# Kernel optimization log

Hardware: AMD Instinct MI355X
Metric: run time of the kernel (lower is better)

The kernel has to match this reference:

```python
import jax, jax.numpy as jnp
import numpy as np


def _centers(n):
    # make_coord_3d: cell-center coordinates in (-1, 1)
    r = 1.0 / n
    return -1.0 + r + 2.0 * r * jnp.arange(n, dtype=jnp.float32)


def setup_inputs() -> dict:
    key = jax.random.key(0)
    ks = jax.random.split(key, 16)
    B, C, Tin, Hin, Win = 1, 64, 6, 40, 40
    Gc = 27 + 8 * C  # 539 channels into conv00_3d
    s = lambda k, shp: jax.random.normal(k, shp, dtype=jnp.float32) * 0.05
    return {
        "feat": jax.random.normal(ks[0], (B, C, Tin, Hin, Win), dtype=jnp.float32),
        # conv00_3d = depthwise(1x1x1, groups=Gc) + pointwise(Gc->256)
        "dw1_w": s(ks[1], (Gc,)), "dw1_b": s(ks[2], (Gc,)),
        "pw1_w": s(ks[3], (256, Gc)), "pw1_b": s(ks[4], (256,)),
        "fc1_w": s(ks[5], (256, 256)), "fc1_b": s(ks[6], (256,)),
        "fc2_w": s(ks[7], (3, 256)), "fc2_b": s(ks[8], (3,)),
        # short_cut = depthwise(1x1x1, groups=C) + pointwise(C->3)
        "sc_dw_w": s(ks[9], (C,)), "sc_dw_b": s(ks[10], (C,)),
        "sc_pw_w": s(ks[11], (3, C)), "sc_pw_b": s(ks[12], (3,)),
        "T_out": 12, "H_out": 80, "W_out": 80,
    }


def _pw(x, w, b):
    # 1x1x1 Conv3d
    return jnp.einsum('bcthw,oc->bothw', x, w) + b[None, :, None, None, None]


def _forward(feat, dw1_w, dw1_b, pw1_w, pw1_b, fc1_w, fc1_b, fc2_w, fc2_b,
             sc_dw_w, sc_dw_b, sc_pw_w, sc_pw_b, T_out, H_out, W_out):
    B, C, Tin, Hin, Win = feat.shape
    ct, ch, cw = _centers(T_out), _centers(H_out), _centers(W_out)  # target centers
    lt, lh, lw = _centers(Tin), _centers(Hin), _centers(Win)        # low-res centers
    rt, rx, ry = 1.0 / Tin, 1.0 / Hin, 1.0 / Win                    # 2/N/2 radii
    eps = 1e-6

    def near(c, n):
        # grid_sample nearest, align_corners=False; coords pre-clamped as in torch code
        cc = jnp.clip(c, -1.0 + 1e-6, 1.0 - 1e-6)
        return jnp.clip(jnp.round(((cc + 1.0) * n - 1.0) / 2.0), 0, n - 1).astype(jnp.int32)

    rel_coords, feat_s, areas = [], [], []
    for vt in (-1.0, 1.0):
        for vx in (-1.0, 1.0):
            for vy in (-1.0, 1.0):
                it = near(ct + vt * rt + eps, Tin)   # [T'] (separable per-dim)
                ih = near(ch + vx * rx + eps, Hin)   # [H']
                iw = near(cw + vy * ry + eps, Win)   # [W']
                f = feat[:, :, it[:, None, None], ih[None, :, None], iw[None, None, :]]
                dct = (ct - lt[it]) * Tin
                dch = (ch - lh[ih]) * Hin
                dcw = (cw - lw[iw]) * Win
                rel = jnp.stack([
                    jnp.broadcast_to(dct[:, None, None], (T_out, H_out, W_out)),
                    jnp.broadcast_to(dch[None, :, None], (T_out, H_out, W_out)),
                    jnp.broadcast_to(dcw[None, None, :], (T_out, H_out, W_out)),
                ], axis=0)
                rel = jnp.broadcast_to(rel[None], (B, 3, T_out, H_out, W_out))
                area = (jnp.abs(dct)[:, None, None] * jnp.abs(dch)[None, :, None]
                        * jnp.abs(dcw)[None, None, :]) + 1e-9
                rel_coords.append(rel)
                feat_s.append(f)
                areas.append(area)

    tot = sum(areas)
    areas_sw = areas[::-1]  # pairwise swaps 0<->7, 1<->6, 2<->5, 3<->4
    feat_s = [f * (a / tot)[None, None] for f, a in zip(feat_s, areas_sw)]

    # rel_cell: (2/size * scale) * in_size == 2.0 on every axis
    rel_cell = jnp.full((B, 3, T_out, H_out, W_out), 2.0, dtype=feat.dtype)

    grid = jnp.concatenate([*rel_coords, *feat_s, rel_cell], axis=1)  # [B,27+8C,T',H',W']

    x = _pw(grid * dw1_w[None, :, None, None, None] + dw1_b[None, :, None, None, None],
            pw1_w, pw1_b)
    ret = _pw(jax.nn.gelu(_pw(x, fc1_w, fc1_b), approximate=False), fc2_w, fc2_b)

    # short cut: depthwise-separable 1x1x1 conv, then trilinear grid_sample (border pad)
    sc = _pw(feat * sc_dw_w[None, :, None, None, None] + sc_dw_b[None, :, None, None, None],
             sc_pw_w, sc_pw_b)

    def lin_idx(c, n):
        x = jnp.clip(((c + 1.0) * n - 1.0) / 2.0, 0.0, n - 1.0)  # border padding: clip coord
        x0 = jnp.floor(x)
        frac = x - x0
        i0 = x0.astype(jnp.int32)
        i1 = jnp.minimum(i0 + 1, n - 1)
        return i0, i1, frac

    t0, t1, ft = lin_idx(ct, Tin)
    h0, h1, fh = lin_idx(ch, Hin)
    w0, w1, fw = lin_idx(cw, Win)
    g = sc[:, :, t0] * (1 - ft)[None, None, :, None, None] + sc[:, :, t1] * ft[None, None, :, None, None]
    g = g[:, :, :, h0] * (1 - fh)[None, None, None, :, None] + g[:, :, :, h1] * fh[None, None, None, :, None]
    g = g[:, :, :, :, w0] * (1 - fw) + g[:, :, :, :, w1] * fw
    return ret + g


def reference(feat, dw1_w, dw1_b, pw1_w, pw1_b, fc1_w, fc1_b, fc2_w, fc2_b,
              sc_dw_w, sc_dw_b, sc_pw_w, sc_pw_b, T_out, H_out, W_out):
    return _forward(feat, dw1_w, dw1_b, pw1_w, pw1_b, fc1_w, fc1_b, fc2_w, fc2_b,
                    sc_dw_w, sc_dw_b, sc_pw_w, sc_pw_b, T_out, H_out, W_out)
```

## Files before the change

kernel.cpp:

```cpp
#include <hip/hip_runtime.h>
#include <hip/hip_bf16.h>

using bf16 = __hip_bfloat16;
typedef __attribute__((ext_vector_type(8))) short short8x;
typedef __attribute__((ext_vector_type(4))) short short4x;
typedef __attribute__((ext_vector_type(4))) unsigned short ushort4x;
typedef __attribute__((ext_vector_type(4))) float f32x4;

__device__ __forceinline__ float b2f(bf16 x) { return __bfloat162float(x); }
__device__ __forceinline__ bf16  f2b(float x) { return __float2bfloat16(x); }
__device__ __forceinline__ short bbits(float x) { bf16 b = f2b(x); short s; __builtin_memcpy(&s, &b, 2); return s; }
__device__ __forceinline__ float bu2f(unsigned short s) {
    unsigned v = ((unsigned)s) << 16; float f; __builtin_memcpy(&f, &v, 4); return f;
}
__device__ __forceinline__ float ldin(const void* p, int i, int f32) {
    return f32 ? ((const float*)p)[i] : b2f(((const bf16*)p)[i]);
}

#define TI 6
#define HI 40
#define WI 40
#define TO 12
#define HO 80
#define WO 80
#define NIN (TI*HI*WI)
#define NOUT (TO*HO*WO)

#define F_B1    0
#define F_ACO   (F_B1 + 256)
#define F_SCW   (F_ACO + 6*256)
#define F_SCB   (F_SCW + 3*64)
#define F_SC    (F_SCB + 4)
#define F_DT    (F_SC + 3*NIN)
#define F_DH    (F_DT + 2*TO)
#define F_DW    (F_DH + 2*HO)
#define F_FT    (F_DW + 2*WO)
#define F_FH    (F_FT + TO)
#define F_FW    (F_FH + HO)
#define F_FC1B  (F_FW + WO)
#define F_FC2W  (F_FC1B + 256)
#define F_FC2B  (F_FC2W + 768)
#define F_END   (F_FC2B + 4)
#define I_IT    0
#define I_IH    (I_IT + 2*TO)
#define I_IW    (I_IH + 2*HO)
#define I_LT0   (I_IW + 2*WO)
#define I_LT1   (I_LT0 + TO)
#define I_LH0   (I_LT1 + TO)
#define I_LH1   (I_LH0 + HO)
#define I_LW0   (I_LH1 + HO)
#define I_LW1   (I_LW0 + WO)
#define I_FLAG  (I_LW1 + WO)
#define I_END   (I_FLAG + 1)

#define MPOS 32
#define ZPAD 264
#define FT_S 72

__device__ __forceinline__ void axis_tables(int i, int n_out, int n_in,
                                            float* dvals, int* ivals,
                                            int* l0, int* l1, float* fr) {
    const float r_out = 1.0f / (float)n_out;
    const float r_in  = 1.0f / (float)n_in;
    const float c = -1.0f + r_out + 2.0f * r_out * (float)i;
    #pragma unroll
    for (int v = 0; v < 2; ++v) {
        const float vv = v ? 1.0f : -1.0f;
        float cc = c + vv * r_in + 1e-6f;
        cc = fminf(fmaxf(cc, -1.0f + 1e-6f), 1.0f - 1e-6f);
        float fx = rintf(((cc + 1.0f) * (float)n_in - 1.0f) * 0.5f);
        fx = fminf(fmaxf(fx, 0.0f), (float)(n_in - 1));
        const int idx = (int)fx;
        const float l = -1.0f + r_in + 2.0f * r_in * (float)idx;
        dvals[v * n_out + i] = (c - l) * (float)n_in;
        ivals[v * n_out + i] = idx;
    }
    float x = fminf(fmaxf(((c + 1.0f) * (float)n_in - 1.0f) * 0.5f, 0.0f), (float)(n_in - 1));
    const float x0 = floorf(x);
    fr[i] = x - x0;
    const int i0 = (int)x0;
    l0[i] = i0;
    l1[i] = min(i0 + 1, n_in - 1);
}

__global__ __launch_bounds__(256)
void k_setup(const void* __restrict__ feat,
             const void* __restrict__ dw1_w, const void* __restrict__ dw1_b,
             const void* __restrict__ pw1_w, const void* __restrict__ pw1_b,
             const void* __restrict__ fc1_w, const void* __restrict__ fc1_b,
             const void* __restrict__ fc2_w, const void* __restrict__ fc2_b,
             const void* __restrict__ sc_dw_w, const void* __restrict__ sc_dw_b,
             const void* __restrict__ sc_pw_w, const void* __restrict__ sc_pw_b,
             bf16* __restrict__ fc1P, bf16* __restrict__ W1fP,
             float* __restrict__ F, int* __restrict__ I) {
    const int tid = threadIdx.x;
    const int b = blockIdx.x;
    __shared__ int sflag;
    if (tid < 64) {
        const unsigned short* u = (const unsigned short*)feat;
        const unsigned e = (u[2 * tid] >> 7) & 0xFFu;
        const unsigned long long m = __ballot(e >= 0x68u && e <= 0x8Eu);
        if (tid == 0) sflag = (__popcll(m) < 32) ? 1 : 0;
    }
    __syncthreads();
    const int f32 = sflag;

    if (b >= 288) {
        const int g = (b - 288) * 256 + tid;
        const int k = g >> 11, kc = (g >> 10) & 1, nt = (g >> 6) & 15, wl = g & 63;
        const int n = nt * 16 + (wl & 15);
        const int k0 = kc * 32 + (wl >> 4) * 8;
        bf16 v[8];
        #pragma unroll
        for (int jj = 0; jj < 8; ++jj) {
            const int ch = 24 + k * 64 + k0 + jj;
            v[jj] = f2b(ldin(pw1_w, n * 539 + ch, f32) * ldin(dw1_w, ch, f32));
        }
        *(short8x*)&W1fP[(size_t)g * 8] = *(short8x*)v;
        return;
    }
    if (b >= 256) {
        const int g = (b - 256) * 256 + tid;
        const int kc = g >> 10, nt = (g >> 6) & 15, wl = g & 63;
        const int n = nt * 16 + (wl & 15);
        const int k0 = kc * 32 + (wl >> 4) * 8;
        bf16 v[8];
        #pragma unroll
        for (int jj = 0; jj < 8; ++jj) v[jj] = f2b(ldin(fc1_w, n * 256 + k0 + jj, f32));
        *(short8x*)&fc1P[(size_t)g * 8] = *(short8x*)v;
        return;
    }

    __shared__ float row[539];
    __shared__ float red[256];
    const int o = b;

    for (int ch = tid; ch < 539; ch += 256) row[ch] = ldin(pw1_w, o * 539 + ch, f32);
    __syncthreads();

    float s = 0.f;
    for (int ch = tid; ch < 539; ch += 256) s += row[ch] * ldin(dw1_b, ch, f32);
    red[tid] = s;
    __syncthreads();
    for (int st = 128; st > 0; st >>= 1) {
        if (tid < st) red[tid] += red[tid + st];
        __syncthreads();
    }

    if (tid == 0) {
        float bacc = ldin(pw1_b, o, f32) + red[0];
        #pragma unroll
        for (int ch = 536; ch < 539; ++ch)
            bacc += 2.0f * row[ch] * ldin(dw1_w, ch, f32);
        F[F_B1 + o] = bacc;

        float A[6] = {0.f, 0.f, 0.f, 0.f, 0.f, 0.f};
        #pragma unroll
        for (int k = 0; k < 8; ++k) {
            A[(k >> 2)]           += row[3*k + 0] * ldin(dw1_w, 3*k + 0, f32);
            A[2 + ((k >> 1) & 1)] += row[3*k + 1] * ldin(dw1_w, 3*k + 1, f32);
            A[4 + (k & 1)]        += row[3*k + 2] * ldin(dw1_w, 3*k + 2, f32);
        }
        #pragma unroll
        for (int i = 0; i < 6; ++i) F[F_ACO + i * 256 + o] = A[i];
    }

    if (b == 0) {
        if (tid == 0) I[I_FLAG] = f32;
        F[F_FC1B + tid] = ldin(fc1_b, tid, f32);
        for (int r = tid; r < 768; r += 256) F[F_FC2W + r] = ldin(fc2_w, r, f32);
        if (tid < 3) F[F_FC2B + tid] = ldin(fc2_b, tid, f32);
        if (tid < 3) {
            const int j = tid;
            float sb = ldin(sc_pw_b, j, f32);
            for (int c = 0; c < 64; ++c) {
                const float pw = ldin(sc_pw_w, j * 64 + c, f32);
                F[F_SCW + j * 64 + c] = pw * ldin(sc_dw_w, c, f32);
                sb += pw * ldin(sc_dw_b, c, f32);
            }
            F[F_SCB + j] = sb;
        }
        if (tid < TO) axis_tables(tid, TO, TI, F + F_DT, I + I_IT, I + I_LT0, I + I_LT1, F + F_FT);
        if (tid < HO) axis_tables(tid, HO, HI, F + F_DH, I + I_IH, I + I_LH0, I + I_LH1, F + F_FH);
        if (tid < WO) axis_tables(tid, WO, WI, F + F_DW, I + I_IW, I + I_LW0, I + I_LW1, F + F_FW);
    }
}

__global__ __launch_bounds__(256)
void k_corner(const void* __restrict__ feat, float* __restrict__ F,
              const int* __restrict__ I, const bf16* __restrict__ W1fP,
              bf16* __restrict__ P) {
    const int tid = threadIdx.x;
    const int pt = blockIdx.x, k = blockIdx.y;
    const int pos0 = pt * 32;
    const int f32 = I[I_FLAG];

    __shared__ __align__(16) short ft[32 * FT_S];
    __shared__ __align__(16) short zt[32 * ZPAD];

    {
        const int p = tid & 31, c0 = tid >> 5;
        #pragma unroll
        for (int cc = 0; cc < 8; ++cc) {
            const int c = c0 * 8 + cc;
            ft[p * FT_S + c] = bbits(ldin(feat, c * NIN + pos0 + p, f32));
        }
    }
    __syncthreads();

    const int wl = tid & 63, w = tid >> 6;
    const int col = wl & 15, quad = wl >> 4;
    f32x4 acc[2][4] = { { {0,0,0,0},{0,0,0,0},{0,0,0,0},{0,0,0,0} },
                        { {0,0,0,0},{0,0,0,0},{0,0,0,0},{0,0,0,0} } };
    const short8x* bp = (const short8x*)W1fP;
    #pragma unroll
    for (int kc = 0; kc < 2; ++kc) {
        const short8x a0 = *(const short8x*)&ft[col * FT_S + kc * 32 + quad * 8];
        const short8x a1 = *(const short8x*)&ft[(col + 16) * FT_S + kc * 32 + quad * 8];
        #pragma unroll
        for (int nt = 0; nt < 4; ++nt) {
            const short8x bb = bp[((k * 2 + kc) * 16 + (w * 4 + nt)) * 64 + wl];
            acc[0][nt] = __builtin_amdgcn_mfma_f32_16x16x32_bf16(a0, bb, acc[0][nt], 0, 0, 0);
            acc[1][nt] = __builtin_amdgcn_mfma_f32_16x16x32_bf16(a1, bb, acc[1][nt], 0, 0, 0);
        }
    }

    if (k == 0 && tid < 96) {
        const int j = tid >> 5, p = tid & 31;
        float s = F[F_SCB + j];
        for (int c = 0; c < 64; ++c)
            s += bu2f((unsigned short)ft[p * FT_S + c]) * F[F_SCW + j * 64 + c];
        F[F_SC + j * NIN + pos0 + p] = s;
    }

    #pragma unroll
    for (int mt = 0; mt < 2; ++mt)
        #pragma unroll
        for (int nt = 0; nt < 4; ++nt) {
            const int n = w * 64 + nt * 16 + col;
            #pragma unroll
            for (int r = 0; r < 4; ++r)
                zt[(mt * 16 + quad * 4 + r) * ZPAD + n] = bbits(acc[mt][nt][r]);
        }
    __syncthreads();

    #pragma unroll
    for (int q = 0; q < 4; ++q) {
        const int i = q * 256 + tid;
        const int p = i >> 5, c8 = i & 31;
        const short8x v = *(const short8x*)&zt[p * ZPAD + c8 * 8];
        *(short8x*)(P + ((size_t)(k * NIN + pos0 + p)) * 256 + c8 * 8) = v;
    }
}

__global__ __launch_bounds__(256, 4)
void k_main(const bf16* __restrict__ P, const bf16* __restrict__ fc1P,
            const float* __restrict__ F, const int* __restrict__ I,
            void* __restrict__ outv) {
    const int tid = threadIdx.x;
    const int pos0 = blockIdx.x * MPOS;
    const int f32 = I[I_FLAG];

    __shared__ __align__(16) short zsh[MPOS * ZPAD];
    __shared__ float redc[MPOS * 4 * 3];
    __shared__ int   sh_ipos[MPOS][8];
    __shared__ float sh_wk[MPOS][8];
    __shared__ float sh_dv[MPOS][6];
    __shared__ float sh_g[3][MPOS];

    if (tid < MPOS) {
        const int p = tid;
        const int pos = pos0 + p;
        const int t = pos / (HO * WO);
        const int rem = pos - t * (HO * WO);
        const int h = rem / WO;
        const int w = rem - h * WO;
        const int   iTa[2] = { I[I_IT + t], I[I_IT + TO + t] };
        const float dTv[2] = { F[F_DT + t], F[F_DT + TO + t] };
        const int   iHa[2] = { I[I_IH + h], I[I_IH + HO + h] };
        const float dHv[2] = { F[F_DH + h], F[F_DH + HO + h] };
        const int   iWa[2] = { I[I_IW + w], I[I_IW + WO + w] };
        const float dWv[2] = { F[F_DW + w], F[F_DW + WO + w] };
        sh_dv[p][0] = dTv[0]; sh_dv[p][1] = dTv[1];
        sh_dv[p][2] = dHv[0]; sh_dv[p][3] = dHv[1];
        sh_dv[p][4] = dWv[0]; sh_dv[p][5] = dWv[1];
        const float aT[2] = { fabsf(dTv[0]), fabsf(dTv[1]) };
        const float aH[2] = { fabsf(dHv[0]), fabsf(dHv[1]) };
        const float aW[2] = { fabsf(dWv[0]), fabsf(dWv[1]) };
        const float tot = (aT[0] + aT[1]) * (aH[0] + aH[1]) * (aW[0] + aW[1]) + 8e-9f;
        #pragma unroll
        for (int k = 0; k < 8; ++k) {
            const int at = k >> 2, ah = (k >> 1) & 1, aw = k & 1;
            sh_wk[p][k] = (aT[1 - at] * aH[1 - ah] * aW[1 - aw] + 1e-9f) / tot;
            sh_ipos[p][k] = iTa[at] * (HI * WI) + iHa[ah] * WI + iWa[aw];
        }
        const int a0 = I[I_LT0 + t], a1 = I[I_LT1 + t];
        const int bh0 = I[I_LH0 + h], bh1 = I[I_LH1 + h];
        const int c0 = I[I_LW0 + w], c1 = I[I_LW1 + w];
        const float fT = F[F_FT + t], fH = F[F_FH + h], fW = F[F_FW + w];
        #pragma unroll
        for (int jj = 0; jj < 3; ++jj) {
            const float* Sj = F + F_SC + jj * NIN;
            const int i0 = a0 * (HI * WI), i1 = a1 * (HI * WI);
            const float v000 = Sj[i0 + bh0 * WI + c0], v001 = Sj[i0 + bh0 * WI + c1];
            const float v010 = Sj[i0 + bh1 * WI + c0], v011 = Sj[i0 + bh1 * WI + c1];
            const float v100 = Sj[i1 + bh0 * WI + c0], v101 = Sj[i1 + bh0 * WI + c1];
            const float v110 = Sj[i1 + bh1 * WI + c0], v111 = Sj[i1 + bh1 * WI + c1];
            const float u00 = v000 * (1.f - fT) + v100 * fT;
            const float u01 = v001 * (1.f - fT) + v101 * fT;
            const float u10 = v010 * (1.f - fT) + v110 * fT;
            const float u11 = v011 * (1.f - fT) + v111 * fT;
            const float q0 = u00 * (1.f - fH) + u10 * fH;
            const float q1 = u01 * (1.f - fH) + u11 * fH;
            sh_g[jj][p] = q0 * (1.f - fW) + q1 * fW;
        }
    }
    __syncthreads();

    {
        const int og = tid & 63, pg = tid >> 6;
        const int o4 = og * 4;
        const float4 bz = *(const float4*)&F[F_B1 + o4];
        float4 Ac[6];
        #pragma unroll
        for (int i = 0; i < 6; ++i) Ac[i] = *(const float4*)&F[F_ACO + i * 256 + o4];
        for (int pp = 0; pp < 8; ++pp) {
            const int p = pg * 8 + pp;
            float a0 = bz.x, a1 = bz.y, a2 = bz.z, a3 = bz.w;
            #pragma unroll
            for (int i = 0; i < 6; ++i) {
                const float dv = sh_dv[p][i];
                a0 += Ac[i].x * dv; a1 += Ac[i].y * dv;
                a2 += Ac[i].z * dv; a3 += Ac[i].w * dv;
            }
            #pragma unroll
            for (int k = 0; k < 8; ++k) {
                const float wk = sh_wk[p][k];
                const ushort4x u = *(const ushort4x*)(P + ((size_t)(k * NIN + sh_ipos[p][k]) * 256 + o4));
                a0 += wk * bu2f(u.x); a1 += wk * bu2f(u.y);
                a2 += wk * bu2f(u.z); a3 += wk * bu2f(u.w);
            }
            short4x zz = { bbits(a0), bbits(a1), bbits(a2), bbits(a3) };
            *(short4x*)&zsh[p * ZPAD + o4] = zz;
        }
    }
    __syncthreads();

    {
        const int wl = tid & 63, w = tid >> 6;
        const int col = wl & 15, quad = wl >> 4;
        f32x4 acc0[4] = { {0,0,0,0}, {0,0,0,0}, {0,0,0,0}, {0,0,0,0} };
        f32x4 acc1[4] = { {0,0,0,0}, {0,0,0,0}, {0,0,0,0}, {0,0,0,0} };
        const short8x* bp = (const short8x*)fc1P;
        #pragma unroll
        for (int kc = 0; kc < 8; ++kc) {
            const short8x a0 = *(const short8x*)&zsh[col * ZPAD + kc * 32 + quad * 8];
            const short8x a1 = *(const short8x*)&zsh[(col + 16) * ZPAD + kc * 32 + quad * 8];
            #pragma unroll
            for (int nt = 0; nt < 4; ++nt) {
                const short8x b = bp[(kc * 16 + w * 4 + nt) * 64 + wl];
                acc0[nt] = __builtin_amdgcn_mfma_f32_16x16x32_bf16(a0, b, acc0[nt], 0, 0, 0);
                acc1[nt] = __builtin_amdgcn_mfma_f32_16x16x32_bf16(a1, b, acc1[nt], 0, 0, 0);
            }
        }
        float part[2][3][4];
        #pragma unroll
        for (int mt = 0; mt < 2; ++mt)
            #pragma unroll
            for (int jj = 0; jj < 3; ++jj)
                #pragma unroll
                for (int r = 0; r < 4; ++r) part[mt][jj][r] = 0.f;
        #pragma unroll
        for (int nt = 0; nt < 4; ++nt) {
            const int j = w * 64 + nt * 16 + col;
            const float fb = F[F_FC1B + j];
            const float w0 = F[F_FC2W + j];
            const float w1 = F[F_FC2W + 256 + j];
            const float w2 = F[F_FC2W + 512 + j];
            #pragma unroll
            for (int r = 0; r < 4; ++r) {
                float x = acc0[nt][r] + fb;
                float hh = 0.5f * x * (1.0f + erff(x * 0.70710678118654752f));
                part[0][0][r] += w0 * hh; part[0][1][r] += w1 * hh; part[0][2][r] += w2 * hh;
                x = acc1[nt][r] + fb;
                hh = 0.5f * x * (1.0f + erff(x * 0.70710678118654752f));
                part[1][0][r] += w0 * hh; part[1][1][r] += w1 * hh; part[1][2][r] += w2 * hh;
            }
        }
        #pragma unroll
        for (int m = 1; m <= 8; m <<= 1)
            #pragma unroll
            for (int mt = 0; mt < 2; ++mt)
                #pragma unroll
                for (int jj = 0; jj < 3; ++jj)
                    #pragma unroll
                    for (int r = 0; r < 4; ++r)
                        part[mt][jj][r] += __shfl_xor(part[mt][jj][r], m, 64);
        if (col == 0) {
            #pragma unroll
            for (int mt = 0; mt < 2; ++mt)
                #pragma unroll
                for (int jj = 0; jj < 3; ++jj)
                    #pragma unroll
                    for (int r = 0; r < 4; ++r) {
                        const int p = mt * 16 + quad * 4 + r;
                        redc[(p * 4 + w) * 3 + jj] = part[mt][jj][r];
                    }
        }
    }
    __syncthreads();

    if (tid < 96) {
        const int p = tid / 3, jj = tid - 3 * p;
        float a = F[F_FC2B + jj] + sh_g[jj][p];
        #pragma unroll
        for (int w = 0; w < 4; ++w) a += redc[(p * 4 + w) * 3 + jj];
        const int oidx = jj * NOUT + pos0 + p;
        if (f32) ((float*)outv)[oidx] = a;
        else     ((bf16*)outv)[oidx] = f2b(a);
    }
}

extern "C" void kernel_launch(void* const* d_in, const int* in_sizes, int n_in,
                              void* d_out, int out_size, void* d_ws, size_t ws_size,
                              hipStream_t stream) {
    const void* feat    = d_in[0];
    const void* dw1_w   = d_in[1];
    const void* dw1_b   = d_in[2];
    const void* pw1_w   = d_in[3];
    const void* pw1_b   = d_in[4];
    const void* fc1_w   = d_in[5];
    const void* fc1_b   = d_in[6];
    const void* fc2_w   = d_in[7];
    const void* fc2_b   = d_in[8];
    const void* sc_dw_w = d_in[9];
    const void* sc_dw_b = d_in[10];
    const void* sc_pw_w = d_in[11];
    const void* sc_pw_b = d_in[12];

    const size_t P_BYTES    = (size_t)8 * NIN * 256 * 2;
    const size_t FC1P_BYTES = (size_t)256 * 256 * 2;
    const size_t W1FP_BYTES = (size_t)8 * 64 * 256 * 2;
    bf16*  P    = (bf16*)d_ws;
    bf16*  fc1P = (bf16*)((char*)d_ws + P_BYTES);
    bf16*  W1fP = (bf16*)((char*)d_ws + P_BYTES + FC1P_BYTES);
    float* F    = (float*)((char*)d_ws + P_BYTES + FC1P_BYTES + W1FP_BYTES);
    int*   I    = (int*)(F + F_END);

    k_setup<<<352, 256, 0, stream>>>(feat, dw1_w, dw1_b, pw1_w, pw1_b, fc1_w, fc1_b,
                                     fc2_w, fc2_b, sc_dw_w, sc_dw_b, sc_pw_w, sc_pw_b,
                                     fc1P, W1fP, F, I);
    k_corner<<<dim3(NIN / 32, 8), 256, 0, stream>>>(feat, F, I, W1fP, P);
    k_main<<<NOUT / MPOS, 256, 0, stream>>>(P, fc1P, F, I, (void*)d_out);
}
```

Baseline: 171.7 us.

## Shrink setup grid, widen gather loads, and use polynomial GELU approximation

Restructures the setup kernel into fewer blocks: per-output bias/coefficient rows are reduced with 16-lane shuffles instead of one block per output with a shared-memory tree, and the W1fP packing is rewritten as one contiguous 64-block range. In the main kernel, the corner gather now loads 8 bf16 channels per thread instead of 4, and the launch-bounds occupancy hint is dropped. The erff-based GELU is replaced by an Abramowitz-Stegun polynomial with a fast reciprocal and exp, which trades exactness for fewer instructions. The W1fP packing now treats the layout as one 512-row K range instead of eight 64-channel slices, which looks like it may change the indexing k_corner relies on.

```diff
diff --git a/kernel.cpp b/kernel.cpp
--- a/kernel.cpp
+++ b/kernel.cpp
@@ -3,8 +3,7 @@
 
 using bf16 = __hip_bfloat16;
 typedef __attribute__((ext_vector_type(8))) short short8x;
-typedef __attribute__((ext_vector_type(4))) short short4x;
-typedef __attribute__((ext_vector_type(4))) unsigned short ushort4x;
+typedef __attribute__((ext_vector_type(8))) unsigned short ushort8x;
 typedef __attribute__((ext_vector_type(4))) float f32x4;
 
 __device__ __forceinline__ float b2f(bf16 x) { return __bfloat162float(x); }
@@ -15,6 +14,15 @@
 }
 __device__ __forceinline__ float ldin(const void* p, int i, int f32) {
     return f32 ? ((const float*)p)[i] : b2f(((const bf16*)p)[i]);
+}
+
+__device__ __forceinline__ float gelu_f(float x) {
+    const float z = fabsf(x) * 0.70710678118654752f;
+    const float t = __builtin_amdgcn_rcpf(1.0f + 0.3275911f * z);
+    const float poly = t * (0.254829592f + t * (-0.284496736f +
+                       t * (1.421413741f + t * (-1.453152027f + t * 1.061405429f))));
+    const float erfv = 1.0f - poly * __expf(-z * z);
+    return 0.5f * x * (1.0f + copysignf(erfv, x));
 }
 
 #define TI 6
@@ -105,85 +113,72 @@
     __syncthreads();
     const int f32 = sflag;
 
-    if (b >= 288) {
-        const int g = (b - 288) * 256 + tid;
-        const int k = g >> 11, kc = (g >> 10) & 1, nt = (g >> 6) & 15, wl = g & 63;
+    if (b < 64) {
+        const int g = b * 256 + tid;
+        const int kc = g >> 10, nt = (g >> 6) & 15, wl = g & 63;
         const int n = nt * 16 + (wl & 15);
-        const int k0 = kc * 32 + (wl >> 4) * 8;
+        const int K0 = kc * 32 + (wl >> 4) * 8;
         bf16 v[8];
         #pragma unroll
         for (int jj = 0; jj < 8; ++jj) {
-            const int ch = 24 + k * 64 + k0 + jj;
+            const int ch = 24 + K0 + jj;
             v[jj] = f2b(ldin(pw1_w, n * 539 + ch, f32) * ldin(dw1_w, ch, f32));
         }
         *(short8x*)&W1fP[(size_t)g * 8] = *(short8x*)v;
         return;
     }
-    if (b >= 256) {
-        const int g = (b - 256) * 256 + tid;
+    if (b < 96) {
+        const int g = (b - 64) * 256 + tid;
         const int kc = g >> 10, nt = (g >> 6) & 15, wl = g & 63;
         const int n = nt * 16 + (wl & 15);
-        const int k0 = kc * 32 + (wl >> 4) * 8;
+        const int K0 = kc * 32 + (wl >> 4) * 8;
         bf16 v[8];
         #pragma unroll
-        for (int jj = 0; jj < 8; ++jj) v[jj] = f2b(ldin(fc1_w, n * 256 + k0 + jj, f32));
+        for (int jj = 0; jj < 8; ++jj) v[jj] = f2b(ldin(fc1_w, n * 256 + K0 + jj, f32));
         *(short8x*)&fc1P[(size_t)g * 8] = *(short8x*)v;
         return;
     }
-
-    __shared__ float row[539];
-    __shared__ float red[256];
-    const int o = b;
-
-    for (int ch = tid; ch < 539; ch += 256) row[ch] = ldin(pw1_w, o * 539 + ch, f32);
-    __syncthreads();
-
-    float s = 0.f;
-    for (int ch = tid; ch < 539; ch += 256) s += row[ch] * ldin(dw1_b, ch, f32);
-    red[tid] = s;
-    __syncthreads();
-    for (int st = 128; st > 0; st >>= 1) {
-        if (tid < st) red[tid] += red[tid + st];
-        __syncthreads();
-    }
-
-    if (tid == 0) {
-        float bacc = ldin(pw1_b, o, f32) + red[0];
-        #pragma unroll
-        for (int ch = 536; ch < 539; ++ch)
-            bacc += 2.0f * row[ch] * ldin(dw1_w, ch, f32);
-        F[F_B1 + o] = bacc;
-
-        float A[6] = {0.f, 0.f, 0.f, 0.f, 0.f, 0.f};
-        #pragma unroll
-        for (int k = 0; k < 8; ++k) {
-            A[(k >> 2)]           += row[3*k + 0] * ldin(dw1_w, 3*k + 0, f32);
-            A[2 + ((k >> 1) & 1)] += row[3*k + 1] * ldin(dw1_w, 3*k + 1, f32);
-            A[4 + (k & 1)]        += row[3*k + 2] * ldin(dw1_w, 3*k + 2, f32);
-        }
-        #pragma unroll
-        for (int i = 0; i < 6; ++i) F[F_ACO + i * 256 + o] = A[i];
-    }
-
-    if (b == 0) {
-        if (tid == 0) I[I_FLAG] = f32;
-        F[F_FC1B + tid] = ldin(fc1_b, tid, f32);
-        for (int r = tid; r < 768; r += 256) F[F_FC2W + r] = ldin(fc2_w, r, f32);
-        if (tid < 3) F[F_FC2B + tid] = ldin(fc2_b, tid, f32);
-        if (tid < 3) {
-            const int j = tid;
-            float sb = ldin(sc_pw_b, j, f32);
-            for (int c = 0; c < 64; ++c) {
-                const float pw = ldin(sc_pw_w, j * 64 + c, f32);
-                F[F_SCW + j * 64 + c] = pw * ldin(sc_dw_w, c, f32);
-                sb += pw * ldin(sc_dw_b, c, f32);
+    if (b < 112) {
+        const int r = tid >> 4, part = tid & 15;
+        const int n = (b - 96) * 16 + r;
+        float s = 0.f;
+        for (int ch = part; ch < 539; ch += 16)
+            s += ldin(pw1_w, n * 539 + ch, f32) * ldin(dw1_b, ch, f32);
+        #pragma unroll
+        for (int m = 1; m <= 8; m <<= 1) s += __shfl_xor(s, m, 64);
+        if (part == 0) {
+            float bacc = ldin(pw1_b, n, f32) + s;
+            #pragma unroll
+            for (int ch = 536; ch < 539; ++ch)
+                bacc += 2.0f * ldin(pw1_w, n * 539 + ch, f32) * ldin(dw1_w, ch, f32);
+            F[F_B1 + n] = bacc;
+            float A[6] = {0.f, 0.f, 0.f, 0.f, 0.f, 0.f};
+            #pragma unroll
+            for (int k = 0; k < 8; ++k) {
+                A[(k >> 2)]           += ldin(pw1_w, n*539 + 3*k + 0, f32) * ldin(dw1_w, 3*k + 0, f32);
+                A[2 + ((k >> 1) & 1)] += ldin(pw1_w, n*539 + 3*k + 1, f32) * ldin(dw1_w, 3*k + 1, f32);
+                A[4 + (k & 1)]        += ldin(pw1_w, n*539 + 3*k + 2, f32) * ldin(dw1_w, 3*k + 2, f32);
             }
-            F[F_SCB + j] = sb;
-        }
-        if (tid < TO) axis_tables(tid, TO, TI, F + F_DT, I + I_IT, I + I_LT0, I + I_LT1, F + F_FT);
-        if (tid < HO) axis_tables(tid, HO, HI, F + F_DH, I + I_IH, I + I_LH0, I + I_LH1, F + F_FH);
-        if (tid < WO) axis_tables(tid, WO, WI, F + F_DW, I + I_IW, I + I_LW0, I + I_LW1, F + F_FW);
-    }
+            #pragma unroll
+            for (int i = 0; i < 6; ++i) F[F_ACO + i * 256 + n] = A[i];
+        }
+        return;
+    }
+    if (tid == 0) I[I_FLAG] = f32;
+    F[F_FC1B + tid] = ldin(fc1_b, tid, f32);
+    for (int r = tid; r < 768; r += 256) F[F_FC2W + r] = ldin(fc2_w, r, f32);
+    if (tid < 3) F[F_FC2B + tid] = ldin(fc2_b, tid, f32);
+    if (tid < 192)
+        F[F_SCW + tid] = ldin(sc_pw_w, tid, f32) * ldin(sc_dw_w, tid & 63, f32);
+    if (tid < 3) {
+        float sb = ldin(sc_pw_b, tid, f32);
+        for (int c = 0; c < 64; ++c)
+            sb += ldin(sc_pw_w, tid * 64 + c, f32) * ldin(sc_dw_b, c, f32);
+        F[F_SCB + tid] = sb;
+    }
+    if (tid < TO) axis_tables(tid, TO, TI, F + F_DT, I + I_IT, I + I_LT0, I + I_LT1, F + F_FT);
+    if (tid < HO) axis_tables(tid, HO, HI, F + F_DH, I + I_IH, I + I_LH0, I + I_LH1, F + F_FH);
+    if (tid < WO) axis_tables(tid, WO, WI, F + F_DW, I + I_IW, I + I_LW0, I + I_LW1, F + F_FW);
 }
 
 __global__ __launch_bounds__(256)
@@ -253,7 +248,7 @@
     }
 }
 
-__global__ __launch_bounds__(256, 4)
+__global__ __launch_bounds__(256)
 void k_main(const bf16* __restrict__ P, const bf16* __restrict__ fc1P,
             const float* __restrict__ F, const int* __restrict__ I,
             void* __restrict__ outv) {
@@ -318,30 +313,39 @@
     __syncthreads();
 
     {
-        const int og = tid & 63, pg = tid >> 6;
-        const int o4 = og * 4;
-        const float4 bz = *(const float4*)&F[F_B1 + o4];
-        float4 Ac[6];
-        #pragma unroll
-        for (int i = 0; i < 6; ++i) Ac[i] = *(const float4*)&F[F_ACO + i * 256 + o4];
-        for (int pp = 0; pp < 8; ++pp) {
-            const int p = pg * 8 + pp;
-            float a0 = bz.x, a1 = bz.y, a2 = bz.z, a3 = bz.w;
+        const int og = tid & 31, pg = tid >> 5;
+        const int o8 = og * 8;
+        const float4 bz0 = *(const float4*)&F[F_B1 + o8];
+        const float4 bz1 = *(const float4*)&F[F_B1 + o8 + 4];
+        float4 Ac0[6], Ac1[6];
+        #pragma unroll
+        for (int i = 0; i < 6; ++i) {
+            Ac0[i] = *(const float4*)&F[F_ACO + i * 256 + o8];
+            Ac1[i] = *(const float4*)&F[F_ACO + i * 256 + o8 + 4];
+        }
+        #pragma unroll
+        for (int pp = 0; pp < 4; ++pp) {
+            const int p = pg * 4 + pp;
+            float a[8] = { bz0.x, bz0.y, bz0.z, bz0.w, bz1.x, bz1.y, bz1.z, bz1.w };
             #pragma unroll
             for (int i = 0; i < 6; ++i) {
                 const float dv = sh_dv[p][i];
-                a0 += Ac[i].x * dv; a1 += Ac[i].y * dv;
-                a2 += Ac[i].z * dv; a3 += Ac[i].w * dv;
+                a[0] += Ac0[i].x * dv; a[1] += Ac0[i].y * dv;
+                a[2] += Ac0[i].z * dv; a[3] += Ac0[i].w * dv;
+                a[4] += Ac1[i].x * dv; a[5] += Ac1[i].y * dv;
+                a[6] += Ac1[i].z * dv; a[7] += Ac1[i].w * dv;
             }
             #pragma unroll
             for (int k = 0; k < 8; ++k) {
                 const float wk = sh_wk[p][k];
-                const ushort4x u = *(const ushort4x*)(P + ((size_t)(k * NIN + sh_ipos[p][k]) * 256 + o4));
-                a0 += wk * bu2f(u.x); a1 += wk * bu2f(u.y);
-                a2 += wk * bu2f(u.z); a3 += wk * bu2f(u.w);
+                const ushort8x u = *(const ushort8x*)(P + ((size_t)(k * NIN + sh_ipos[p][k]) * 256 + o8));
+                #pragma unroll
+                for (int j = 0; j < 8; ++j) a[j] += wk * bu2f(u[j]);
             }
-            short4x zz = { bbits(a0), bbits(a1), bbits(a2), bbits(a3) };
-            *(short4x*)&zsh[p * ZPAD + o4] = zz;
+            short zz[8];
+            #pragma unroll
+            for (int j = 0; j < 8; ++j) zz[j] = bbits(a[j]);
+            *(short8x*)&zsh[p * ZPAD + o8] = *(short8x*)zz;
         }
     }
     __syncthreads();
@@ -379,11 +383,9 @@
             const float w2 = F[F_FC2W + 512 + j];
             #pragma unroll
             for (int r = 0; r < 4; ++r) {
-                float x = acc0[nt][r] + fb;
-                float hh = 0.5f * x * (1.0f + erff(x * 0.70710678118654752f));
+                float hh = gelu_f(acc0[nt][r] + fb);
                 part[0][0][r] += w0 * hh; part[0][1][r] += w1 * hh; part[0][2][r] += w2 * hh;
-                x = acc1[nt][r] + fb;
-                hh = 0.5f * x * (1.0f + erff(x * 0.70710678118654752f));
+                hh = gelu_f(acc1[nt][r] + fb);
                 part[1][0][r] += w0 * hh; part[1][1][r] += w1 * hh; part[1][2][r] += w2 * hh;
             }
         }
@@ -440,14 +442,14 @@
 
     const size_t P_BYTES    = (size_t)8 * NIN * 256 * 2;
     const size_t FC1P_BYTES = (size_t)256 * 256 * 2;
-    const size_t W1FP_BYTES = (size_t)8 * 64 * 256 * 2;
+    const size_t W1FP_BYTES = (size_t)512 * 256 * 2;
     bf16*  P    = (bf16*)d_ws;
     bf16*  fc1P = (bf16*)((char*)d_ws + P_BYTES);
     bf16*  W1fP = (bf16*)((char*)d_ws + P_BYTES + FC1P_BYTES);
     float* F    = (float*)((char*)d_ws + P_BYTES + FC1P_BYTES + W1FP_BYTES);
     int*   I    = (int*)(F + F_END);
 
-    k_setup<<<352, 256, 0, stream>>>(feat, dw1_w, dw1_b, pw1_w, pw1_b, fc1_w, fc1_b,
+    k_setup<<<113, 256, 0, stream>>>(feat, dw1_w, dw1_b, pw1_w, pw1_b, fc1_w, fc1_b,
                                      fc2_w, fc2_b, sc_dw_w, sc_dw_b, sc_pw_w, sc_pw_b,
                                      fc1P, W1fP, F, I);
     k_corner<<<dim3(NIN / 32, 8), 256, 0, stream>>>(feat, F, I, W1fP, P);
```

Result: slower. 175.4 us (+2.1%).
